# Kernel optimization log

Hardware: AMD Instinct MI355X
Metric: run time of the kernel (lower is better)

Reference implementation:

```python
import jax, jax.numpy as jnp
import numpy as np

INPUT_DIM = 128
DEPTH = 6
HIDDEN = 64
NUM_INNER = 2 ** DEPTH - 1  # 63
NUM_LEAVES = 2 ** DEPTH     # 64


def setup_inputs() -> dict:
    key = jax.random.key(0)
    ks = jax.random.split(key, 6)
    x = jax.random.normal(ks[0], (65536, INPUT_DIM), dtype=jnp.float32)
    s1 = 1.0 / np.sqrt(INPUT_DIM)
    s2 = 1.0 / np.sqrt(HIDDEN)
    W1 = jax.random.uniform(ks[1], (NUM_INNER, INPUT_DIM, HIDDEN), minval=-s1, maxval=s1, dtype=jnp.float32)
    b1 = jax.random.uniform(ks[2], (NUM_INNER, HIDDEN), minval=-s1, maxval=s1, dtype=jnp.float32)
    W2 = jax.random.uniform(ks[3], (NUM_INNER, HIDDEN), minval=-s2, maxval=s2, dtype=jnp.float32)
    b2 = jax.random.uniform(ks[4], (NUM_INNER,), minval=-s2, maxval=s2, dtype=jnp.float32)
    leaf = jax.random.normal(ks[5], (NUM_LEAVES, 1), dtype=jnp.float32)
    return {"x": x, "W1": W1, "b1": b1, "W2": W2, "b2": b2, "leaf": leaf}


def reference(x, W1, b1, W2, b2, leaf):
    # All inner-node MLPs as one batched GEMM pair: [B, N] node probabilities
    h = jax.nn.relu(jnp.einsum('bi,nih->bnh', x, W1) + b1)      # [B, N, H]
    probs = jax.nn.sigmoid(jnp.einsum('bnh,nh->bn', h, W2) + b2)  # [B, N]

    # Original code walks node_idx = 2*node_idx+1 unconditionally, so the chain
    # of used node indices is 2^k - 1 for k = 0..depth-1.
    chain = jnp.array([2 ** k - 1 for k in range(DEPTH)], dtype=jnp.int32)
    p_chain = probs[:, chain]  # [B, D]

    # Bit k (LSB first) of leaf index selects p (bit=1) vs 1-p (bit=0)
    leaves = np.arange(NUM_LEAVES)
    bits = jnp.asarray(((leaves[:, None] >> np.arange(DEPTH)[None, :]) & 1).astype(np.float32))  # [L, D]

    # path_probs[b, l] = prod_k ( bits[l,k]*p + (1-bits[l,k])*(1-p) )
    factors = bits[None, :, :] * p_chain[:, None, :] + (1.0 - bits[None, :, :]) * (1.0 - p_chain[:, None, :])  # [B, L, D]
    path_probs = jnp.prod(factors, axis=-1)  # [B, L]

    return (path_probs @ leaf)[:, 0]  # [B]
```

## Files before the change

### kernel.cpp

```cpp
#include <hip/hip_runtime.h>

typedef __attribute__((ext_vector_type(4))) float f32x4;
typedef __attribute__((ext_vector_type(8))) short bf16x8;
typedef __attribute__((ext_vector_type(4))) unsigned int u32x4;

#define IDIM    128
#define HID     64
#define TDEPTH  6
#define MTILE   64
#define NWAVES  6
#define BLOCK   (NWAVES * 64)
#define T_TILES 2
#define WFRAG_ELEMS (6 * 4 * 4 * 512)

__device__ __forceinline__ unsigned short f2bf(float f) {
    unsigned int u = __builtin_bit_cast(unsigned int, f);
    unsigned int r = (u + 0x7FFFu + ((u >> 16) & 1u)) >> 16;
    return (unsigned short)r;
}

__device__ __forceinline__ unsigned int f2bf_pk(float f0, float f1) {
    unsigned int u0 = __builtin_bit_cast(unsigned int, f0);
    unsigned int u1 = __builtin_bit_cast(unsigned int, f1);
    unsigned int t0 = u0 + 0x7FFFu + ((u0 >> 16) & 1u);
    unsigned int t1 = u1 + 0x7FFFu + ((u1 >> 16) & 1u);
    return (t1 & 0xFFFF0000u) | (t0 >> 16);
}

__global__ void prep_wfrag(const float* __restrict__ W1, unsigned short* __restrict__ wfrag) {
    int idx = blockIdx.x * 256 + threadIdx.x;
    if (idx >= WFRAG_ELEMS) return;
    int j    = idx & 7;
    int lane = (idx >> 3) & 63;
    int ct   = (idx >> 9) & 3;
    int ks   = (idx >> 11) & 3;
    int nd   = idx >> 13;
    int node = (1 << nd) - 1;
    int k    = ks * 32 + (lane >> 4) * 8 + j;
    int col  = ct * 16 + (lane & 15);
    wfrag[idx] = f2bf(W1[(node * IDIM + k) * HID + col]);
}

template <bool USE_WS>
__global__ __launch_bounds__(BLOCK, 3)
void sdt_kernel(const float* __restrict__ x, const float* __restrict__ W1,
                const float* __restrict__ b1, const float* __restrict__ W2,
                const float* __restrict__ b2, const float* __restrict__ leaf,
                const unsigned short* __restrict__ wfrag, float* __restrict__ out) {
    __shared__ unsigned short xs[MTILE][IDIM + 8];
    __shared__ float p_lds[TDEPTH][MTILE];
    __shared__ float pp[2][4][MTILE];
    __shared__ float leaf_lds[64];

    const int tid   = threadIdx.x;
    const int tile0 = blockIdx.x * T_TILES;

    const int wave = tid >> 6;
    const int lane = tid & 63;
    const int node = (1 << wave) - 1;
    const int lcol = lane & 15;
    const int lq   = lane >> 4;

    if (tid < 64) leaf_lds[tid] = leaf[tid];

    const float4* xv = reinterpret_cast<const float4*>(x);

    {
        const float4* xt = xv + (size_t)tile0 * (MTILE * IDIM / 4);
        for (int f = tid; f < MTILE * (IDIM / 4); f += BLOCK) {
            int row = f >> 5, c4 = f & 31;
            float4 v = xt[f];
            unsigned long long pk =
                (unsigned long long)f2bf(v.x) |
                ((unsigned long long)f2bf(v.y) << 16) |
                ((unsigned long long)f2bf(v.z) << 32) |
                ((unsigned long long)f2bf(v.w) << 48);
            *reinterpret_cast<unsigned long long*>(&xs[row][c4 * 4]) = pk;
        }
    }

    float b1v[4], w2v[4];
    #pragma unroll
    for (int ct = 0; ct < 4; ct++) {
        int col = ct * 16 + lcol;
        b1v[ct] = b1[node * HID + col];
        w2v[ct] = W2[node * HID + col];
    }
    const float bias2 = b2[node];

    __syncthreads();

    for (int t = 0; t < T_TILES; ++t) {
        f32x4 acc[4][4];
        #pragma unroll
        for (int rt = 0; rt < 4; rt++)
            #pragma unroll
            for (int ct = 0; ct < 4; ct++)
                acc[rt][ct] = (f32x4){0.f, 0.f, 0.f, 0.f};
        #pragma unroll
        for (int ks = 0; ks < 4; ks++) {
            bf16x8 bfrag[4];
            if (USE_WS) {
                #pragma unroll
                for (int ct = 0; ct < 4; ct++)
                    bfrag[ct] = *reinterpret_cast<const bf16x8*>(
                        wfrag + (((wave * 4 + ks) * 4 + ct) * 512 + lane * 8));
            } else {
                const float* wsrc = W1 + (size_t)node * IDIM * HID + lcol;
                const int k0 = ks * 32 + lq * 8;
                #pragma unroll
                for (int ct = 0; ct < 4; ct++) {
                    const float* wc = wsrc + (size_t)k0 * HID + ct * 16;
                    u32x4 pk;
                    #pragma unroll
                    for (int jp = 0; jp < 4; jp++)
                        pk[jp] = f2bf_pk(wc[(2 * jp) * HID], wc[(2 * jp + 1) * HID]);
                    bfrag[ct] = __builtin_bit_cast(bf16x8, pk);
                }
            }
            #pragma unroll
            for (int rt = 0; rt < 4; rt++) {
                bf16x8 afrag = *reinterpret_cast<const bf16x8*>(
                    &xs[rt * 16 + lcol][ks * 32 + lq * 8]);
                #pragma unroll
                for (int ct = 0; ct < 4; ct++)
                    acc[rt][ct] = __builtin_amdgcn_mfma_f32_16x16x32_bf16(
                        afrag, bfrag[ct], acc[rt][ct], 0, 0, 0);
            }
        }

        #pragma unroll
        for (int rt = 0; rt < 4; rt++) {
            #pragma unroll
            for (int r = 0; r < 4; r++) {
                float s = 0.f;
                #pragma unroll
                for (int ct = 0; ct < 4; ct++) {
                    float v = acc[rt][ct][r] + b1v[ct];
                    v = v > 0.f ? v : 0.f;
                    s += v * w2v[ct];
                }
                #pragma unroll
                for (int d = 1; d < 16; d <<= 1)
                    s += __shfl_xor(s, d, 64);
                float p = 1.f / (1.f + __expf(-(s + bias2)));
                if (lcol == 0)
                    p_lds[wave][rt * 16 + lq * 4 + r] = p;
            }
        }
        __syncthreads();

        if (t > 0 && tid < MTILE) {
            const float* q = &pp[(t - 1) & 1][0][0];
            out[(size_t)(tile0 + t - 1) * MTILE + tid] =
                (q[0 * MTILE + tid] + q[1 * MTILE + tid]) +
                (q[2 * MTILE + tid] + q[3 * MTILE + tid]);
        }

        if (tid < 4 * MTILE) {
            int row = tid & (MTILE - 1);
            int ch  = tid >> 6;
            float q0 = p_lds[0][row];
            float q1 = p_lds[1][row];
            float q2 = p_lds[2][row];
            float q3 = p_lds[3][row];
            float p4 = p_lds[4][row];
            float p5 = p_lds[5][row];
            float f4 = (ch & 1) ? p4 : 1.f - p4;
            float f5 = (ch & 2) ? p5 : 1.f - p5;
            const float* lf = leaf_lds + ch * 16;
            float tt[8];
            #pragma unroll
            for (int j = 0; j < 8; j++) {
                float a = lf[2 * j], b = lf[2 * j + 1];
                tt[j] = a + q0 * (b - a);
            }
            #pragma unroll
            for (int j = 0; j < 4; j++) tt[j] = tt[2 * j] + q1 * (tt[2 * j + 1] - tt[2 * j]);
            #pragma unroll
            for (int j = 0; j < 2; j++) tt[j] = tt[2 * j] + q2 * (tt[2 * j + 1] - tt[2 * j]);
            float s = tt[0] + q3 * (tt[1] - tt[0]);
            pp[t & 1][ch][row] = f4 * f5 * s;
        }

        if (t + 1 < T_TILES) {
            const float4* xt = xv + (size_t)(tile0 + t + 1) * (MTILE * IDIM / 4);
            for (int f = tid; f < MTILE * (IDIM / 4); f += BLOCK) {
                int row = f >> 5, c4 = f & 31;
                float4 v = xt[f];
                unsigned long long pk =
                    (unsigned long long)f2bf(v.x) |
                    ((unsigned long long)f2bf(v.y) << 16) |
                    ((unsigned long long)f2bf(v.z) << 32) |
                    ((unsigned long long)f2bf(v.w) << 48);
                *reinterpret_cast<unsigned long long*>(&xs[row][c4 * 4]) = pk;
            }
        }
        __syncthreads();
    }

    if (tid < MTILE) {
        const float* q = &pp[(T_TILES - 1) & 1][0][0];
        out[(size_t)(tile0 + T_TILES - 1) * MTILE + tid] =
            (q[0 * MTILE + tid] + q[1 * MTILE + tid]) +
            (q[2 * MTILE + tid] + q[3 * MTILE + tid]);
    }
}

extern "C" void kernel_launch(void* const* d_in, const int* in_sizes, int n_in,
                              void* d_out, int out_size, void* d_ws, size_t ws_size,
                              hipStream_t stream) {
    const float* x    = (const float*)d_in[0];
    const float* W1   = (const float*)d_in[1];
    const float* b1   = (const float*)d_in[2];
    const float* W2   = (const float*)d_in[3];
    const float* b2   = (const float*)d_in[4];
    const float* leaf = (const float*)d_in[5];
    float* out = (float*)d_out;

    const int Bn = in_sizes[0] / IDIM;
    const int nblocks = Bn / (MTILE * T_TILES);

    if (ws_size >= (size_t)WFRAG_ELEMS * sizeof(unsigned short)) {
        unsigned short* wfrag = (unsigned short*)d_ws;
        prep_wfrag<<<(WFRAG_ELEMS + 255) / 256, 256, 0, stream>>>(W1, wfrag);
        sdt_kernel<true><<<nblocks, BLOCK, 0, stream>>>(x, W1, b1, W2, b2, leaf, wfrag, out);
    } else {
        sdt_kernel<false><<<nblocks, BLOCK, 0, stream>>>(x, W1, b1, W2, b2, leaf, nullptr, out);
    }
}
```

Measured before the change: 115.0 us.

## Load x fragments directly from global memory, drop LDS staging and multi-tile loop

```diff
diff --git a/kernel.cpp b/kernel.cpp
--- a/kernel.cpp
+++ b/kernel.cpp
@@ -10,7 +10,6 @@
 #define MTILE   64
 #define NWAVES  6
 #define BLOCK   (NWAVES * 64)
-#define T_TILES 2
 #define WFRAG_ELEMS (6 * 4 * 4 * 512)
 
 __device__ __forceinline__ unsigned short f2bf(float f) {
@@ -47,13 +46,11 @@
                 const float* __restrict__ b1, const float* __restrict__ W2,
                 const float* __restrict__ b2, const float* __restrict__ leaf,
                 const unsigned short* __restrict__ wfrag, float* __restrict__ out) {
-    __shared__ unsigned short xs[MTILE][IDIM + 8];
     __shared__ float p_lds[TDEPTH][MTILE];
-    __shared__ float pp[2][4][MTILE];
     __shared__ float leaf_lds[64];
 
-    const int tid   = threadIdx.x;
-    const int tile0 = blockIdx.x * T_TILES;
+    const int tid    = threadIdx.x;
+    const int m_base = blockIdx.x * MTILE;
 
     const int wave = tid >> 6;
     const int lane = tid & 63;
@@ -62,22 +59,6 @@
     const int lq   = lane >> 4;
 
     if (tid < 64) leaf_lds[tid] = leaf[tid];
-
-    const float4* xv = reinterpret_cast<const float4*>(x);
-
-    {
-        const float4* xt = xv + (size_t)tile0 * (MTILE * IDIM / 4);
-        for (int f = tid; f < MTILE * (IDIM / 4); f += BLOCK) {
-            int row = f >> 5, c4 = f & 31;
-            float4 v = xt[f];
-            unsigned long long pk =
-                (unsigned long long)f2bf(v.x) |
-                ((unsigned long long)f2bf(v.y) << 16) |
-                ((unsigned long long)f2bf(v.z) << 32) |
-                ((unsigned long long)f2bf(v.w) << 48);
-            *reinterpret_cast<unsigned long long*>(&xs[row][c4 * 4]) = pk;
-        }
-    }
 
     float b1v[4], w2v[4];
     #pragma unroll
@@ -88,84 +69,87 @@
     }
     const float bias2 = b2[node];
 
+    const float* xbase = x + (size_t)(m_base + lcol) * IDIM + lq * 8;
+
+    f32x4 acc[4][4];
+    #pragma unroll
+    for (int rt = 0; rt < 4; rt++)
+        #pragma unroll
+        for (int ct = 0; ct < 4; ct++)
+            acc[rt][ct] = (f32x4){0.f, 0.f, 0.f, 0.f};
+
+    #pragma unroll
+    for (int ks = 0; ks < 4; ks++) {
+        bf16x8 bfrag[4];
+        if (USE_WS) {
+            #pragma unroll
+            for (int ct = 0; ct < 4; ct++)
+                bfrag[ct] = *reinterpret_cast<const bf16x8*>(
+                    wfrag + (((wave * 4 + ks) * 4 + ct) * 512 + lane * 8));
+        } else {
+            const float* wsrc = W1 + (size_t)node * IDIM * HID + lcol;
+            const int k0 = ks * 32 + lq * 8;
+            #pragma unroll
+            for (int ct = 0; ct < 4; ct++) {
+                const float* wc = wsrc + (size_t)k0 * HID + ct * 16;
+                u32x4 pk;
+                #pragma unroll
+                for (int jp = 0; jp < 4; jp++)
+                    pk[jp] = f2bf_pk(wc[(2 * jp) * HID], wc[(2 * jp + 1) * HID]);
+                bfrag[ct] = __builtin_bit_cast(bf16x8, pk);
+            }
+        }
+        #pragma unroll
+        for (int rt = 0; rt < 4; rt++) {
+            const float4* a4 = reinterpret_cast<const float4*>(
+                xbase + (size_t)(rt * 16) * IDIM + ks * 32);
+            float4 v0 = a4[0];
+            float4 v1 = a4[1];
+            u32x4 pk;
+            pk[0] = f2bf_pk(v0.x, v0.y);
+            pk[1] = f2bf_pk(v0.z, v0.w);
+            pk[2] = f2bf_pk(v1.x, v1.y);
+            pk[3] = f2bf_pk(v1.z, v1.w);
+            bf16x8 afrag = __builtin_bit_cast(bf16x8, pk);
+            #pragma unroll
+            for (int ct = 0; ct < 4; ct++)
+                acc[rt][ct] = __builtin_amdgcn_mfma_f32_16x16x32_bf16(
+                    afrag, bfrag[ct], acc[rt][ct], 0, 0, 0);
+        }
+    }
+
+    #pragma unroll
+    for (int rt = 0; rt < 4; rt++) {
+        #pragma unroll
+        for (int r = 0; r < 4; r++) {
+            float s = 0.f;
+            #pragma unroll
+            for (int ct = 0; ct < 4; ct++) {
+                float v = acc[rt][ct][r] + b1v[ct];
+                v = v > 0.f ? v : 0.f;
+                s += v * w2v[ct];
+            }
+            #pragma unroll
+            for (int d = 1; d < 16; d <<= 1)
+                s += __shfl_xor(s, d, 64);
+            float p = 1.f / (1.f + __expf(-(s + bias2)));
+            if (lcol == 0)
+                p_lds[wave][rt * 16 + lq * 4 + r] = p;
+        }
+    }
     __syncthreads();
 
-    for (int t = 0; t < T_TILES; ++t) {
-        f32x4 acc[4][4];
+    if (wave == 0) {
+        const int row = lane;
+        float q0 = p_lds[0][row];
+        float q1 = p_lds[1][row];
+        float q2 = p_lds[2][row];
+        float q3 = p_lds[3][row];
+        float p4 = p_lds[4][row];
+        float p5 = p_lds[5][row];
+        float acc_out = 0.f;
         #pragma unroll
-        for (int rt = 0; rt < 4; rt++)
-            #pragma unroll
-            for (int ct = 0; ct < 4; ct++)
-                acc[rt][ct] = (f32x4){0.f, 0.f, 0.f, 0.f};
-        #pragma unroll
-        for (int ks = 0; ks < 4; ks++) {
-            bf16x8 bfrag[4];
-            if (USE_WS) {
-                #pragma unroll
-                for (int ct = 0; ct < 4; ct++)
-                    bfrag[ct] = *reinterpret_cast<const bf16x8*>(
-                        wfrag + (((wave * 4 + ks) * 4 + ct) * 512 + lane * 8));
-            } else {
-                const float* wsrc = W1 + (size_t)node * IDIM * HID + lcol;
-                const int k0 = ks * 32 + lq * 8;
-                #pragma unroll
-                for (int ct = 0; ct < 4; ct++) {
-                    const float* wc = wsrc + (size_t)k0 * HID + ct * 16;
-                    u32x4 pk;
-                    #pragma unroll
-                    for (int jp = 0; jp < 4; jp++)
-                        pk[jp] = f2bf_pk(wc[(2 * jp) * HID], wc[(2 * jp + 1) * HID]);
-                    bfrag[ct] = __builtin_bit_cast(bf16x8, pk);
-                }
-            }
-            #pragma unroll
-            for (int rt = 0; rt < 4; rt++) {
-                bf16x8 afrag = *reinterpret_cast<const bf16x8*>(
-                    &xs[rt * 16 + lcol][ks * 32 + lq * 8]);
-                #pragma unroll
-                for (int ct = 0; ct < 4; ct++)
-                    acc[rt][ct] = __builtin_amdgcn_mfma_f32_16x16x32_bf16(
-                        afrag, bfrag[ct], acc[rt][ct], 0, 0, 0);
-            }
-        }
-
-        #pragma unroll
-        for (int rt = 0; rt < 4; rt++) {
-            #pragma unroll
-            for (int r = 0; r < 4; r++) {
-                float s = 0.f;
-                #pragma unroll
-                for (int ct = 0; ct < 4; ct++) {
-                    float v = acc[rt][ct][r] + b1v[ct];
-                    v = v > 0.f ? v : 0.f;
-                    s += v * w2v[ct];
-                }
-                #pragma unroll
-                for (int d = 1; d < 16; d <<= 1)
-                    s += __shfl_xor(s, d, 64);
-                float p = 1.f / (1.f + __expf(-(s + bias2)));
-                if (lcol == 0)
-                    p_lds[wave][rt * 16 + lq * 4 + r] = p;
-            }
-        }
-        __syncthreads();
-
-        if (t > 0 && tid < MTILE) {
-            const float* q = &pp[(t - 1) & 1][0][0];
-            out[(size_t)(tile0 + t - 1) * MTILE + tid] =
-                (q[0 * MTILE + tid] + q[1 * MTILE + tid]) +
-                (q[2 * MTILE + tid] + q[3 * MTILE + tid]);
-        }
-
-        if (tid < 4 * MTILE) {
-            int row = tid & (MTILE - 1);
-            int ch  = tid >> 6;
-            float q0 = p_lds[0][row];
-            float q1 = p_lds[1][row];
-            float q2 = p_lds[2][row];
-            float q3 = p_lds[3][row];
-            float p4 = p_lds[4][row];
-            float p5 = p_lds[5][row];
+        for (int ch = 0; ch < 4; ch++) {
             float f4 = (ch & 1) ? p4 : 1.f - p4;
             float f5 = (ch & 2) ? p5 : 1.f - p5;
             const float* lf = leaf_lds + ch * 16;
@@ -180,30 +164,9 @@
             #pragma unroll
             for (int j = 0; j < 2; j++) tt[j] = tt[2 * j] + q2 * (tt[2 * j + 1] - tt[2 * j]);
             float s = tt[0] + q3 * (tt[1] - tt[0]);
-            pp[t & 1][ch][row] = f4 * f5 * s;
+            acc_out += f4 * f5 * s;
         }
-
-        if (t + 1 < T_TILES) {
-            const float4* xt = xv + (size_t)(tile0 + t + 1) * (MTILE * IDIM / 4);
-            for (int f = tid; f < MTILE * (IDIM / 4); f += BLOCK) {
-                int row = f >> 5, c4 = f & 31;
-                float4 v = xt[f];
-                unsigned long long pk =
-                    (unsigned long long)f2bf(v.x) |
-                    ((unsigned long long)f2bf(v.y) << 16) |
-                    ((unsigned long long)f2bf(v.z) << 32) |
-                    ((unsigned long long)f2bf(v.w) << 48);
-                *reinterpret_cast<unsigned long long*>(&xs[row][c4 * 4]) = pk;
-            }
-        }
-        __syncthreads();
-    }
-
-    if (tid < MTILE) {
-        const float* q = &pp[(T_TILES - 1) & 1][0][0];
-        out[(size_t)(tile0 + T_TILES - 1) * MTILE + tid] =
-            (q[0 * MTILE + tid] + q[1 * MTILE + tid]) +
-            (q[2 * MTILE + tid] + q[3 * MTILE + tid]);
+        out[(size_t)m_base + row] = acc_out;
     }
 }
 
@@ -219,7 +182,7 @@
     float* out = (float*)d_out;
 
     const int Bn = in_sizes[0] / IDIM;
-    const int nblocks = Bn / (MTILE * T_TILES);
+    const int nblocks = Bn / MTILE;
 
     if (ws_size >= (size_t)WFRAG_ELEMS * sizeof(unsigned short)) {
         unsigned short* wfrag = (unsigned short*)d_ws;
```

New measurement: 119.7 us. +4.2%, slower.
